# Kernel optimization log

Measured on AMD Instinct MI355X. Metric: run time of the kernel, lower is better.

## Reference

```python
import jax, jax.numpy as jnp
import numpy as np

B, L, E, H, V, NC = 64, 256, 300, 128, 50000, 2
NH1, F1 = 8, 8  # GAT layer 1: 8 heads x 8 features; layer 2: 1 head x 1 feature
LRELU = 0.2


def _lstm_dir(x, W, U, b):
    # x: [B, L, E]; W: [4H, E]; U: [4H, H]; b: [4H] (b_ih + b_hh fused)
    Bq, Hq = x.shape[0], U.shape[1]
    def step(carry, xt):
        h, c = carry
        g = xt @ W.T + h @ U.T + b
        i, f, gg, o = jnp.split(g, 4, axis=-1)  # PyTorch gate order i,f,g,o
        c = jax.nn.sigmoid(f) * c + jax.nn.sigmoid(i) * jnp.tanh(gg)
        h = jax.nn.sigmoid(o) * jnp.tanh(c)
        return (h, c), h
    h0 = jnp.zeros((Bq, Hq), x.dtype)
    _, hs = jax.lax.scan(step, (h0, h0), jnp.swapaxes(x, 0, 1))
    return jnp.swapaxes(hs, 0, 1)  # [B, L, H]


def bilstm(x, Wf, Uf, bf, Wb, Ub, bb):
    hf = _lstm_dir(x, Wf, Uf, bf)
    hb = _lstm_dir(x[:, ::-1], Wb, Ub, bb)[:, ::-1]
    return jnp.concatenate([hf, hb], axis=-1)  # [B, L, 2H]


def gat_layer(x, W, a_src, a_trg, bias, n_heads, f_out, concat, elu_act):
    # Dense equivalent of GAT IMP3 on a fully-connected graph (edge (s,t): src=s, trg=t).
    Bq, Lq, _ = x.shape
    proj = (x @ W.T).reshape(Bq, Lq, n_heads, f_out)        # [B,L,NH,F]
    s_src = jnp.einsum('blhf,hf->blh', proj, a_src)          # [B,L,NH]
    s_trg = jnp.einsum('blhf,hf->blh', proj, a_trg)
    sc = jax.nn.leaky_relu(s_src[:, :, None, :] + s_trg[:, None, :, :], LRELU)  # [B,S,T,NH]
    m = jnp.max(sc, axis=(1, 2, 3), keepdims=True)           # global max per graph (as in IMP3)
    e = jnp.exp(sc - m)
    A = e / (jnp.sum(e, axis=1, keepdims=True) + 1e-16)      # softmax over sources per target
    out = jnp.einsum('bsth,bshf->bthf', A, proj)             # scatter-aggregate to targets
    if concat:
        out = out.reshape(Bq, Lq, n_heads * f_out)
    else:
        out = out.mean(axis=2)
    out = out + bias
    if elu_act:
        out = jax.nn.elu(out)
    return out, A


def setup_inputs() -> dict:
    key = jax.random.key(0)
    ks = jax.random.split(key, 20)
    n = lambda k, shape, s=0.05: (jax.random.normal(k, shape, jnp.float32) * s)
    return {
        'input_ids': jax.random.randint(ks[0], (B, L), 0, V, jnp.int32),
        'attention_mask': jnp.ones((B, L), bool),
        'emb': n(ks[1], (V, E), 0.1),
        'Wih_f': n(ks[2], (4 * H, E)), 'Whh_f': n(ks[3], (4 * H, H)), 'b_f': jnp.zeros((4 * H,), jnp.float32),
        'Wih_b': n(ks[4], (4 * H, E)), 'Whh_b': n(ks[5], (4 * H, H)), 'b_b': jnp.zeros((4 * H,), jnp.float32),
        'g1_W': n(ks[6], (NH1 * F1, 2 * H)), 'g1_src': n(ks[7], (NH1, F1), 0.1), 'g1_trg': n(ks[8], (NH1, F1), 0.1), 'g1_b': jnp.zeros((NH1 * F1,), jnp.float32),
        'g2_W': n(ks[9], (1, NH1 * F1)), 'g2_src': n(ks[10], (1, 1), 0.1), 'g2_trg': n(ks[11], (1, 1), 0.1), 'g2_b': jnp.zeros((1,), jnp.float32),
        'ctx': n(ks[12], (L, 1), 0.1),
        'lin_W': n(ks[13], (B, 2 * H)), 'lin_b': jnp.zeros((B,), jnp.float32),
        'out_W': n(ks[14], (NC, B)), 'out_b': jnp.zeros((NC,), jnp.float32),
    }


def reference(input_ids, attention_mask, emb, Wih_f, Whh_f, b_f, Wih_b, Whh_b, b_b,
              g1_W, g1_src, g1_trg, g1_b, g2_W, g2_src, g2_trg, g2_b,
              ctx, lin_W, lin_b, out_W, out_b):
    x = emb[input_ids]                                   # [B,L,E] (dropout = eval no-op)
    h_seq = bilstm(x, Wih_f, Whh_f, b_f, Wih_b, Whh_b, b_b)  # [B,L,2H]
    h1, _ = gat_layer(h_seq, g1_W, g1_src, g1_trg, g1_b, NH1, F1, True, True)
    _, A2 = gat_layer(h1, g2_W, g2_src, g2_trg, g2_b, 1, 1, False, False)
    att2 = A2[..., 0]                                    # [B, src, trg] == att.view(-1, 2H) rows
    att = jnp.einsum('bst,t->bs', att2, ctx[:, 0])       # mm with context_vector
    att = jnp.where(attention_mask, att, -jnp.inf)
    att = jax.nn.softmax(att, axis=1)                    # [B,L]
    pooled = jnp.max(h_seq * att[..., None], axis=1)     # [B,2H]
    hcl = jax.nn.relu(pooled @ lin_W.T + lin_b)
    logits = hcl @ out_W.T + out_b                       # [B,NC]
    return (logits, att)
```

## Files before the change

kernel.cpp:

```cpp
#include <hip/hip_runtime.h>
#include <math.h>
#include <stdint.h>

#define Bq 64
#define Lq 256
#define Eq 300
#define Hq 128
#define MQ (Bq*Lq)
#define AST 320

#define LRELU_S 0.2f

__device__ __forceinline__ float lrelu(float x) { return x > 0.f ? x : LRELU_S * x; }

typedef short short8 __attribute__((ext_vector_type(8)));
typedef float f32x4v __attribute__((ext_vector_type(4)));

__device__ __forceinline__ unsigned short f2bf(float x) {
  unsigned u = __float_as_uint(x);
  u += 0x7FFFu + ((u >> 16) & 1u);
  return (unsigned short)(u >> 16);
}
__device__ __forceinline__ float bf2f(unsigned short h) {
  return __uint_as_float(((unsigned)h) << 16);
}

__device__ __forceinline__ void cv4(float4 v, unsigned short* dh, unsigned short* dl) {
  unsigned short h0 = f2bf(v.x), h1 = f2bf(v.y), h2 = f2bf(v.z), h3 = f2bf(v.w);
  unsigned short l0 = f2bf(v.x - bf2f(h0)), l1 = f2bf(v.y - bf2f(h1));
  unsigned short l2 = f2bf(v.z - bf2f(h2)), l3 = f2bf(v.w - bf2f(h3));
  uint2 ph; ph.x = (unsigned)h0 | ((unsigned)h1 << 16); ph.y = (unsigned)h2 | ((unsigned)h3 << 16);
  uint2 pl; pl.x = (unsigned)l0 | ((unsigned)l1 << 16); pl.y = (unsigned)l2 | ((unsigned)l3 << 16);
  *(uint2*)dh = ph;
  *(uint2*)dl = pl;
}

__global__ __launch_bounds__(256) void gather_conv_kernel(
    const float* __restrict__ emb, const int* __restrict__ ids,
    unsigned short* __restrict__ Agh, unsigned short* __restrict__ Agl)
{
  const int JOBS = MQ * 80;
  for (int j = blockIdx.x * blockDim.x + threadIdx.x; j < JOBS;
       j += gridDim.x * blockDim.x) {
    int row = j / 80, c = j - row * 80;
    size_t off = (size_t)row * AST + c * 4;
    if (c < 75) {
      float4 v = *(const float4*)(emb + (size_t)ids[row] * Eq + c * 4);
      cv4(v, Agh + off, Agl + off);
    } else {
      *(uint2*)(Agh + off) = make_uint2(0u, 0u);
      *(uint2*)(Agl + off) = make_uint2(0u, 0u);
    }
  }
}

__global__ __launch_bounds__(256) void conv_w_kernel(
    const float* __restrict__ Wf, const float* __restrict__ Wb,
    const float* __restrict__ g1_W,
    unsigned short* __restrict__ Wbh, unsigned short* __restrict__ Wbl,
    unsigned short* __restrict__ g1h, unsigned short* __restrict__ g1l)
{
  const int J1 = 1024 * 80;
  const int J2 = 64 * 64;
  for (int j = blockIdx.x * blockDim.x + threadIdx.x; j < J1 + J2;
       j += gridDim.x * blockDim.x) {
    if (j < J1) {
      int row = j / 80, c = j - row * 80;
      size_t off = (size_t)row * AST + c * 4;
      if (c < 75) {
        const float* src = (row < 512) ? (Wf + (size_t)row * 300)
                                       : (Wb + (size_t)(row - 512) * 300);
        float4 v = *(const float4*)(src + c * 4);
        cv4(v, Wbh + off, Wbl + off);
      } else {
        *(uint2*)(Wbh + off) = make_uint2(0u, 0u);
        *(uint2*)(Wbl + off) = make_uint2(0u, 0u);
      }
    } else {
      int j2 = j - J1;
      int row = j2 >> 6, c = j2 & 63;
      size_t off = (size_t)row * 256 + c * 4;
      float4 v = *(const float4*)(g1_W + off);
      cv4(v, g1h + off, g1l + off);
    }
  }
}

__global__ __launch_bounds__(256) void gemm_gates_mfma(
    const unsigned short* __restrict__ Agh, const unsigned short* __restrict__ Agl,
    const unsigned short* __restrict__ Wbh, const unsigned short* __restrict__ Wbl,
    const float* __restrict__ bf, const float* __restrict__ bb_,
    float* __restrict__ C)
{
  __shared__ __align__(16) short Ah[128 * 32];
  __shared__ __align__(16) short Al[128 * 32];
  __shared__ __align__(16) short Bh[128 * 32];
  __shared__ __align__(16) short Bl[128 * 32];

  int tid = threadIdx.x;
  int row0 = blockIdx.x * 128;
  int col0 = blockIdx.y * 128;
  const float* bias = (col0 < 512) ? bf : bb_;
  int wcol0 = col0 & 511;

  int l  = tid & 63, wv = tid >> 6;
  int wm = wv >> 1,  wn = wv & 1;
  int kq = l >> 4,   rl = l & 15;

  f32x4v acc[4][4] = {};

  for (int k0 = 0; k0 < 300; k0 += 32) {
    #pragma unroll
    for (int p = 0; p < 4; ++p) {
      int idx = p * 256 + tid;
      int row = idx >> 3, c4 = idx & 7;
      int gk = k0 + c4 * 4;
      int chunk = (c4 >> 1) ^ ((row >> 2) & 3);
      int off = row * 32 + chunk * 8 + (c4 & 1) * 4;
      size_t ao = (size_t)(row0 + row) * AST + gk;
      *(uint2*)&Ah[off] = *(const uint2*)(Agh + ao);
      *(uint2*)&Al[off] = *(const uint2*)(Agl + ao);
      size_t bo = (size_t)(col0 + row) * AST + gk;
      *(uint2*)&Bh[off] = *(const uint2*)(Wbh + bo);
      *(uint2*)&Bl[off] = *(const uint2*)(Wbl + bo);
    }
    __syncthreads();

    short8 ah[4], al_[4], bh[4], bl[4];
    #pragma unroll
    for (int f = 0; f < 4; ++f) {
      int ar = wm * 64 + f * 16 + rl;
      int ac = kq ^ ((ar >> 2) & 3);
      ah[f]  = *(const short8*)&Ah[ar * 32 + ac * 8];
      al_[f] = *(const short8*)&Al[ar * 32 + ac * 8];
      int br = wn * 64 + f * 16 + rl;
      int bc = kq ^ ((br >> 2) & 3);
      bh[f]  = *(const short8*)&Bh[br * 32 + bc * 8];
      bl[f]  = *(const short8*)&Bl[br * 32 + bc * 8];
    }
    #pragma unroll
    for (int fm = 0; fm < 4; ++fm)
      #pragma unroll
      for (int fn = 0; fn < 4; ++fn) {
        acc[fm][fn] = __builtin_amdgcn_mfma_f32_16x16x32_bf16(ah[fm],  bh[fn], acc[fm][fn], 0, 0, 0);
        acc[fm][fn] = __builtin_amdgcn_mfma_f32_16x16x32_bf16(ah[fm],  bl[fn], acc[fm][fn], 0, 0, 0);
        acc[fm][fn] = __builtin_amdgcn_mfma_f32_16x16x32_bf16(al_[fm], bh[fn], acc[fm][fn], 0, 0, 0);
      }
    __syncthreads();
  }

  int fq = l >> 4;
  #pragma unroll
  for (int fm = 0; fm < 4; ++fm) {
    #pragma unroll
    for (int fn = 0; fn < 4; ++fn) {
      int gr = row0 + wm * 64 + fm * 16 + fq * 4;
      int lc = wn * 64 + fn * 16 + rl;
      float bsv = bias[wcol0 + lc];
      #pragma unroll
      for (int i = 0; i < 4; ++i)
        C[(size_t)(gr + i) * 1024 + col0 + lc] = acc[fm][fn][i] + bsv;
    }
  }
}

__global__ __launch_bounds__(256) void gemm_proj_mfma(
    const unsigned short* __restrict__ Hbh, const unsigned short* __restrict__ Hbl,
    const unsigned short* __restrict__ g1h, const unsigned short* __restrict__ g1l,
    float* __restrict__ C)
{
  __shared__ __align__(16) short Ah[128 * 32];
  __shared__ __align__(16) short Al[128 * 32];
  __shared__ __align__(16) short Bh[64 * 32];
  __shared__ __align__(16) short Bl[64 * 32];

  int tid = threadIdx.x;
  int row0 = blockIdx.x * 128;

  int l  = tid & 63, wv = tid >> 6;
  int wm = wv >> 1,  wn = wv & 1;
  int kq = l >> 4,   rl = l & 15;

  f32x4v acc[4][2] = {};

  for (int k0 = 0; k0 < 256; k0 += 32) {
    #pragma unroll
    for (int p = 0; p < 4; ++p) {
      int idx = p * 256 + tid;
      int row = idx >> 3, c4 = idx & 7;
      int gk = k0 + c4 * 4;
      int chunk = (c4 >> 1) ^ ((row >> 2) & 3);
      int off = row * 32 + chunk * 8 + (c4 & 1) * 4;
      size_t ao = (size_t)(row0 + row) * 256 + gk;
      *(uint2*)&Ah[off] = *(const uint2*)(Hbh + ao);
      *(uint2*)&Al[off] = *(const uint2*)(Hbl + ao);
    }
    #pragma unroll
    for (int p = 0; p < 2; ++p) {
      int idx = p * 256 + tid;
      int row = idx >> 3, c4 = idx & 7;
      int gk = k0 + c4 * 4;
      int chunk = (c4 >> 1) ^ ((row >> 2) & 3);
      int off = row * 32 + chunk * 8 + (c4 & 1) * 4;
      size_t bo = (size_t)row * 256 + gk;
      *(uint2*)&Bh[off] = *(const uint2*)(g1h + bo);
      *(uint2*)&Bl[off] = *(const uint2*)(g1l + bo);
    }
    __syncthreads();

    short8 ah[4], al_[4], bh[2], bl[2];
    #pragma unroll
    for (int f = 0; f < 4; ++f) {
      int ar = wm * 64 + f * 16 + rl;
      int ac = kq ^ ((ar >> 2) & 3);
      ah[f]  = *(const short8*)&Ah[ar * 32 + ac * 8];
      al_[f] = *(const short8*)&Al[ar * 32 + ac * 8];
    }
    #pragma unroll
    for (int f = 0; f < 2; ++f) {
      int br = wn * 32 + f * 16 + rl;
      int bc = kq ^ ((br >> 2) & 3);
      bh[f]  = *(const short8*)&Bh[br * 32 + bc * 8];
      bl[f]  = *(const short8*)&Bl[br * 32 + bc * 8];
    }
    #pragma unroll
    for (int fm = 0; fm < 4; ++fm)
      #pragma unroll
      for (int fn = 0; fn < 2; ++fn) {
        acc[fm][fn] = __builtin_amdgcn_mfma_f32_16x16x32_bf16(ah[fm],  bh[fn], acc[fm][fn], 0, 0, 0);
        acc[fm][fn] = __builtin_amdgcn_mfma_f32_16x16x32_bf16(ah[fm],  bl[fn], acc[fm][fn], 0, 0, 0);
        acc[fm][fn] = __builtin_amdgcn_mfma_f32_16x16x32_bf16(al_[fm], bh[fn], acc[fm][fn], 0, 0, 0);
      }
    __syncthreads();
  }

  int fq = l >> 4;
  #pragma unroll
  for (int fm = 0; fm < 4; ++fm) {
    #pragma unroll
    for (int fn = 0; fn < 2; ++fn) {
      int gr = row0 + wm * 64 + fm * 16 + fq * 4;
      int lc = wn * 32 + fn * 16 + rl;
      #pragma unroll
      for (int i = 0; i < 4; ++i)
        C[(size_t)(gr + i) * 64 + lc] = acc[fm][fn][i];
    }
  }
}

#define MVB(s0,s1,s2,s3, u0,u1,u2,u3, off) \
  "s_waitcnt lgkmcnt(5)\n" \
  "v_fmac_f32 v88, v" #s0 ", v" #u0 "\n" \
  "v_fmac_f32 v89, v" #s1 ", v" #u1 "\n" \
  "v_fmac_f32 v90, v" #s2 ", v" #u2 "\n" \
  "v_fmac_f32 v91, v" #s3 ", v" #u3 "\n" \
  "ds_read_b128 v[" #s0 ":" #s3 "], v81 offset:" #off "\n"

#define MVT(n, s0,s1,s2,s3, u0,u1,u2,u3) \
  "s_waitcnt lgkmcnt(" #n ")\n" \
  "v_fmac_f32 v88, v" #s0 ", v" #u0 "\n" \
  "v_fmac_f32 v89, v" #s1 ", v" #u1 "\n" \
  "v_fmac_f32 v90, v" #s2 ", v" #u2 "\n" \
  "v_fmac_f32 v91, v" #s3 ", v" #u3 "\n"

#define ULD(lo,hi,off) \
  "global_load_dwordx4 v[" #lo ":" #hi "], v80, %[ub] offset:" #off "\n"

__global__ __launch_bounds__(512, 1) void lstm_kernel(
    const float* __restrict__ ws_base,
    const float* __restrict__ Uf, const float* __restrict__ Ub,
    float* __restrict__ h_seq,
    unsigned short* __restrict__ Hbh, unsigned short* __restrict__ Hbl)
{
  __shared__ __align__(1024) float h_sh[2][Hq];
  int blk = blockIdx.x;
  int b = blk & 63;
  int dir = blk >> 6;
  int j = threadIdx.x;
  int lane = j & 63;
  int w = j >> 6;
  int gate = (lane >> 4) & 3;
  int hidx = (w << 4) | (lane & 15);
  int row = (gate << 7) | hidx;

  const float* U = dir ? Ub : Uf;
  int tt0 = dir ? (Lq - 1) : 0;

  unsigned uo  = (unsigned)row * (Hq * 4u);
  unsigned go0 = (1024u + (unsigned)(b * Lq + tt0) * 1024u
                  + (unsigned)dir * 512u + (unsigned)row) * 4u;
  unsigned ho0 = ((unsigned)(b * Lq + tt0) * 256u
                  + (unsigned)dir * (unsigned)Hq + (unsigned)hidx) * 4u;
  unsigned hb0 = ((unsigned)(b * Lq + tt0) * 256u
                  + (unsigned)dir * (unsigned)Hq + (unsigned)hidx) * 2u;
  int gd  = dir ? -4096 : 4096;
  int hd  = dir ? -1024 : 1024;
  int hdb = dir ? -512  : 512;

  unsigned lds_base = (unsigned)(uintptr_t)&h_sh[0][0];
  unsigned ldsr0 = lds_base;
  unsigned ldsw0 = lds_base + 512u + (unsigned)hidx * 4u;

  bool isg = (gate == 2);
  float klog = isg ? -2.8853900817779268f : -1.4426950408889634f;
  float mc = isg ? 2.f : 1.f;
  float ac = isg ? -1.f : 0.f;
  int base4 = (lane & 15) * 4;
  int bp0 = base4, bp1 = base4 + 64, bp2 = base4 + 128, bp3 = base4 + 192;

  if (j < Hq) h_sh[0][j] = 0.f;
  __syncthreads();

  asm volatile(
    "v_mov_b32 v80, %[uo]\n"
    "v_mov_b32 v81, %[ldsr0]\n"
    "v_mov_b32 v82, %[ldsw0]\n"
    "v_mov_b32 v83, %[go0]\n"
    "v_mov_b32 v84, %[ho0]\n"
    "v_mov_b32 v74, %[hb0]\n"
    "v_mov_b32 v87, 0\n"
    "s_mov_b32 s90, 0\n"
    ULD(128,131,0)   ULD(132,135,16)  ULD(136,139,32)  ULD(140,143,48)
    ULD(144,147,64)  ULD(148,151,80)  ULD(152,155,96)  ULD(156,159,112)
    ULD(160,163,128) ULD(164,167,144) ULD(168,171,160) ULD(172,175,176)
    ULD(176,179,192) ULD(180,183,208) ULD(184,187,224) ULD(188,191,240)
    ULD(192,195,256) ULD(196,199,272) ULD(200,203,288) ULD(204,207,304)
    ULD(208,211,320) ULD(212,215,336) ULD(216,219,352) ULD(220,223,368)
    ULD(224,227,384) ULD(228,231,400) ULD(232,235,416) ULD(236,239,432)
    ULD(240,243,448) ULD(244,247,464) ULD(248,251,480) ULD(252,255,496)
    "global_load_dword v85, v83, %[wsb]\n"
    "s_waitcnt vmcnt(0)\n"
    "Ltop_%=:\n"
    "v_add_u32 v83, %[gd], v83\n"
    "global_load_dword v86, v83, %[wsb]\n"
    "ds_read_b128 v[100:103], v81\n"
    "ds_read_b128 v[104:107], v81 offset:16\n"
    "ds_read_b128 v[108:111], v81 offset:32\n"
    "ds_read_b128 v[112:115], v81 offset:48\n"
    "ds_read_b128 v[116:119], v81 offset:64\n"
    "ds_read_b128 v[120:123], v81 offset:80\n"
    "v_mov_b32 v88, v85\n"
    "v_mov_b32 v89, 0\n"
    "v_mov_b32 v90, 0\n"
    "v_mov_b32 v91, 0\n"
    MVB(100,101,102,103, 128,129,130,131, 96)
    MVB(104,105,106,107, 132,133,134,135, 112)
    MVB(108,109,110,111, 136,137,138,139, 128)
    MVB(112,113,114,115, 140,141,142,143, 144)
    MVB(116,117,118,119, 144,145,146,147, 160)
    MVB(120,121,122,123, 148,149,150,151, 176)
    MVB(100,101,102,103, 152,153,154,155, 192)
    MVB(104,105,106,107, 156,157,158,159, 208)
    MVB(108,109,110,111, 160,161,162,163, 224)
    MVB(112,113,114,115, 164,165,166,167, 240)
    MVB(116,117,118,119, 168,169,170,171, 256)
    MVB(120,121,122,123, 172,173,174,175, 272)
    MVB(100,101,102,103, 176,177,178,179, 288)
    MVB(104,105,106,107, 180,181,182,183, 304)
    MVB(108,109,110,111, 184,185,186,187, 320)
    MVB(112,113,114,115, 188,189,190,191, 336)
    MVB(116,117,118,119, 192,193,194,195, 352)
    MVB(120,121,122,123, 196,197,198,199, 368)
    MVB(100,101,102,103, 200,201,202,203, 384)
    MVB(104,105,106,107, 204,205,206,207, 400)
    MVB(108,109,110,111, 208,209,210,211, 416)
    MVB(112,113,114,115, 212,213,214,215, 432)
    MVB(116,117,118,119, 216,217,218,219, 448)
    MVB(120,121,122,123, 220,221,222,223, 464)
    MVB(100,101,102,103, 224,225,226,227, 480)
    MVB(104,105,106,107, 228,229,230,231, 496)
    MVT(5, 108,109,110,111, 232,233,234,235)
    MVT(4, 112,113,114,115, 236,237,238,239)
    MVT(3, 116,117,118,119, 240,241,242,243)
    MVT(2, 120,121,122,123, 244,245,246,247)
    MVT(1, 100,101,102,103, 248,249,250,251)
    MVT(0, 104,105,106,107, 252,253,254,255)
    "v_add_f32 v88, v88, v90\n"
    "v_add_f32 v89, v89, v91\n"
    "v_add_f32 v88, v88, v89\n"
    "v_mul_f32 v92, %[klog], v88\n"
    "v_exp_f32 v93, v92\n"
    "s_nop 1\n"
    "v_add_f32 v94, 1.0, v93\n"
    "v_rcp_f32 v95, v94\n"
    "s_nop 1\n"
    "v_fma_f32 v97, v95, %[mc], %[ac]\n"
    "ds_bpermute_b32 v92, %[bp0], v97\n"
    "ds_bpermute_b32 v93, %[bp1], v97\n"
    "ds_bpermute_b32 v94, %[bp2], v97\n"
    "ds_bpermute_b32 v98, %[bp3], v97\n"
    "s_waitcnt lgkmcnt(0)\n"
    "v_mul_f32 v95, v92, v94\n"
    "v_fma_f32 v87, v93, v87, v95\n"
    "v_mul_f32 v92, 0xc038aa3b, v87\n"
    "v_exp_f32 v93, v92\n"
    "s_nop 1\n"
    "v_add_f32 v94, 1.0, v93\n"
    "v_rcp_f32 v95, v94\n"
    "s_nop 1\n"
    "v_fma_f32 v96, v95, 2.0, -1.0\n"
    "v_mul_f32 v96, v98, v96\n"
    "v_bfe_u32 v75, v96, 16, 1\n"
    "v_add_u32 v75, 0x7fff, v75\n"
    "v_add_u32 v76, v96, v75\n"
    "v_lshrrev_b32 v77, 16, v76\n"
    "v_lshlrev_b32 v78, 16, v77\n"
    "v_sub_f32 v78, v96, v78\n"
    "v_bfe_u32 v75, v78, 16, 1\n"
    "v_add_u32 v75, 0x7fff, v75\n"
    "v_add_u32 v79, v78, v75\n"
    "v_lshrrev_b32 v79, 16, v79\n"
    "s_waitcnt vmcnt(0)\n"
    "v_mov_b32 v85, v86\n"
    "ds_write_b32 v82, v96\n"
    "global_store_dword v84, v96, %[hsb]\n"
    "global_store_short v74, v77, %[hbh]\n"
    "global_store_short v74, v79, %[hbl]\n"
    "v_add_u32 v84, %[hd], v84\n"
    "v_add_u32 v74, %[hdb], v74\n"
    "v_xor_b32 v81, 0x200, v81\n"
    "v_xor_b32 v82, 0x200, v82\n"
    "s_waitcnt lgkmcnt(0)\n"
    "s_barrier\n"
    "s_add_u32 s90, s90, 1\n"
    "s_cmp_lt_u32 s90, 256\n"
    "s_cbranch_scc1 Ltop_%=\n"
    "s_waitcnt vmcnt(0) lgkmcnt(0)\n"
    :
    : [wsb]"s"(ws_base), [hsb]"s"(h_seq), [ub]"s"(U),
      [hbh]"s"(Hbh), [hbl]"s"(Hbl),
      [gd]"s"(gd), [hd]"s"(hd), [hdb]"s"(hdb),
      [uo]"v"(uo), [go0]"v"(go0), [ho0]"v"(ho0), [hb0]"v"(hb0),
      [ldsr0]"v"(ldsr0), [ldsw0]"v"(ldsw0),
      [klog]"v"(klog), [mc]"v"(mc), [ac]"v"(ac),
      [bp0]"v"(bp0), [bp1]"v"(bp1), [bp2]"v"(bp2), [bp3]"v"(bp3)
    : "memory", "scc", "s90",
      "v74","v75","v76","v77","v78","v79",
      "v80","v81","v82","v83","v84","v85","v86","v87","v88","v89",
      "v90","v91","v92","v93","v94","v95","v96","v97","v98",
      "v100","v101","v102","v103","v104","v105","v106","v107",
      "v108","v109","v110","v111","v112","v113","v114","v115",
      "v116","v117","v118","v119","v120","v121","v122","v123",
      "v128","v129","v130","v131","v132","v133","v134","v135",
      "v136","v137","v138","v139","v140","v141","v142","v143",
      "v144","v145","v146","v147","v148","v149","v150","v151",
      "v152","v153","v154","v155","v156","v157","v158","v159",
      "v160","v161","v162","v163","v164","v165","v166","v167",
      "v168","v169","v170","v171","v172","v173","v174","v175",
      "v176","v177","v178","v179","v180","v181","v182","v183",
      "v184","v185","v186","v187","v188","v189","v190","v191",
      "v192","v193","v194","v195","v196","v197","v198","v199",
      "v200","v201","v202","v203","v204","v205","v206","v207",
      "v208","v209","v210","v211","v212","v213","v214","v215",
      "v216","v217","v218","v219","v220","v221","v222","v223",
      "v224","v225","v226","v227","v228","v229","v230","v231",
      "v232","v233","v234","v235","v236","v237","v238","v239",
      "v240","v241","v242","v243","v244","v245","v246","v247",
      "v248","v249","v250","v251","v252","v253","v254","v255");
}
#undef MVB
#undef MVT
#undef ULD

__device__ __forceinline__ float block_max_256(float v, volatile float* red) {
  #pragma unroll
  for (int o = 32; o > 0; o >>= 1) v = fmaxf(v, __shfl_xor(v, o, 64));
  int tid = threadIdx.x;
  if ((tid & 63) == 0) red[tid >> 6] = v;
  __syncthreads();
  float r = fmaxf(fmaxf(red[0], red[1]), fmaxf(red[2], red[3]));
  __syncthreads();
  return r;
}
__device__ __forceinline__ float block_sum_256(float v, volatile float* red) {
  #pragma unroll
  for (int o = 32; o > 0; o >>= 1) v += __shfl_xor(v, o, 64);
  int tid = threadIdx.x;
  if ((tid & 63) == 0) red[tid >> 6] = v;
  __syncthreads();
  float r = red[0] + red[1] + red[2] + red[3];
  __syncthreads();
  return r;
}

__global__ __launch_bounds__(256) void gat1_fused_kernel(
    const float* __restrict__ proj1, const float* __restrict__ g1_src,
    const float* __restrict__ g1_trg, const float* __restrict__ g1_b,
    float* __restrict__ h1)
{
  int b = blockIdx.x >> 3;
  int h = blockIdx.x & 7;
  int t = threadIdx.x;
  __shared__ float src_s[Lq], trg_s[Lq];
  __shared__ float proj_s[Lq * 8];
  __shared__ float red[4];

  size_t base = (size_t)b * Lq;
  float pv[8];
  {
    const float4* pr = (const float4*)(proj1 + (base + t) * 64 + h * 8);
    float4 p0 = pr[0], p1 = pr[1];
    pv[0]=p0.x; pv[1]=p0.y; pv[2]=p0.z; pv[3]=p0.w;
    pv[4]=p1.x; pv[5]=p1.y; pv[6]=p1.z; pv[7]=p1.w;
    float4* psh = (float4*)(proj_s + t * 8);
    psh[0] = p0; psh[1] = p1;
  }
  float ss = 0.f, st = 0.f;
  #pragma unroll
  for (int f = 0; f < 8; ++f) {
    ss += pv[f] * g1_src[h * 8 + f];
    st += pv[f] * g1_trg[h * 8 + f];
  }
  src_s[t] = ss;
  trg_s[t] = st;
  __syncthreads();

  float ms = block_max_256(ss, red);
  float mt = block_max_256(st, red);
  float m = lrelu(ms + mt);

  float mytrg = trg_s[t];
  float den = 1e-16f;
  float acc[8] = {};
  for (int s = 0; s < Lq; ++s) {
    float wgt = __expf(lrelu(src_s[s] + mytrg) - m);
    den += wgt;
    const float* ps = proj_s + s * 8;
    #pragma unroll
    for (int f = 0; f < 8; ++f) acc[f] += wgt * ps[f];
  }
  float inv = 1.f / den;
  float* out = h1 + (base + t) * 64 + h * 8;
  #pragma unroll
  for (int f = 0; f < 8; ++f) {
    float v = acc[f] * inv + g1_b[h * 8 + f];
    out[f] = v > 0.f ? v : expm1f(v);
  }
}

__global__ __launch_bounds__(256) void gat2_pool_head_kernel(
    const float* __restrict__ h1, const float* __restrict__ g2_W,
    const float* __restrict__ g2_src, const float* __restrict__ g2_trg,
    const float* __restrict__ ctx, const float* __restrict__ h_seq,
    const float* __restrict__ lin_W, const float* __restrict__ lin_b,
    const float* __restrict__ out_W, const float* __restrict__ out_b,
    float* __restrict__ att_out, float* __restrict__ logits)
{
  int b = blockIdx.x;
  int tid = threadIdx.x;
  __shared__ float w2[64];
  __shared__ float src2[Lq], trg2[Lq], dq[Lq], att_sh[Lq], pool_sh[256];
  __shared__ float red[4];
  __shared__ float part[4][64];
  __shared__ float hcl[64];

  if (tid < 64) w2[tid] = g2_W[tid];
  __syncthreads();

  const float* hr = h1 + ((size_t)b * Lq + tid) * 64;
  float p = 0.f;
  #pragma unroll
  for (int k = 0; k < 64; ++k) p += hr[k] * w2[k];
  float a_s = g2_src[0], a_t = g2_trg[0];
  src2[tid] = p * a_s;
  trg2[tid] = p * a_t;
  __syncthreads();

  float ms = block_max_256(src2[tid], red);
  float mt = block_max_256(trg2[tid], red);
  float m2 = lrelu(ms + mt);

  float mytrg = trg2[tid];
  float d0 = 1e-16f, d1 = 0.f, d2 = 0.f, d3 = 0.f;
  for (int s = 0; s < Lq; s += 4) {
    d0 += __expf(lrelu(src2[s + 0] + mytrg) - m2);
    d1 += __expf(lrelu(src2[s + 1] + mytrg) - m2);
    d2 += __expf(lrelu(src2[s + 2] + mytrg) - m2);
    d3 += __expf(lrelu(src2[s + 3] + mytrg) - m2);
  }
  dq[tid] = ctx[tid] / ((d0 + d1) + (d2 + d3));
  __syncthreads();

  float mysrc = src2[tid];
  float r0 = 0.f, r1 = 0.f, r2 = 0.f, r3 = 0.f;
  for (int t = 0; t < Lq; t += 4) {
    r0 += dq[t + 0] * __expf(lrelu(mysrc + trg2[t + 0]) - m2);
    r1 += dq[t + 1] * __expf(lrelu(mysrc + trg2[t + 1]) - m2);
    r2 += dq[t + 2] * __expf(lrelu(mysrc + trg2[t + 2]) - m2);
    r3 += dq[t + 3] * __expf(lrelu(mysrc + trg2[t + 3]) - m2);
  }
  float raw = (r0 + r1) + (r2 + r3);

  float mr = block_max_256(raw, red);
  float e = __expf(raw - mr);
  float ssum = block_sum_256(e, red);
  float att = e / ssum;
  att_out[(size_t)b * Lq + tid] = att;
  att_sh[tid] = att;
  __syncthreads();

  float pm = -3.4e38f;
  const float* hb = h_seq + (size_t)b * Lq * 256 + tid;
  for (int l = 0; l < Lq; l += 4) {
    float v0 = hb[(size_t)(l + 0) * 256] * att_sh[l + 0];
    float v1 = hb[(size_t)(l + 1) * 256] * att_sh[l + 1];
    float v2 = hb[(size_t)(l + 2) * 256] * att_sh[l + 2];
    float v3 = hb[(size_t)(l + 3) * 256] * att_sh[l + 3];
    pm = fmaxf(pm, fmaxf(fmaxf(v0, v1), fmaxf(v2, v3)));
  }
  pool_sh[tid] = pm;
  __syncthreads();

  {
    int jj = tid & 63, kq = tid >> 6;
    const float* pr = pool_sh + kq * 64;
    const float* wr = lin_W + jj * 256 + kq * 64;
    float d = 0.f;
    #pragma unroll
    for (int k = 0; k < 64; ++k) d += pr[k] * wr[k];
    part[kq][jj] = d;
  }
  __syncthreads();
  if (tid < 64) {
    float v = part[0][tid] + part[1][tid] + part[2][tid] + part[3][tid] + lin_b[tid];
    hcl[tid] = fmaxf(v, 0.f);
  }
  __syncthreads();
  if (tid < 128) {
    int cc = tid >> 6, jj = tid & 63;
    float pp = hcl[jj] * out_W[cc * 64 + jj];
    #pragma unroll
    for (int o = 32; o > 0; o >>= 1) pp += __shfl_xor(pp, o, 64);
    if (jj == 0) logits[b * 2 + cc] = pp + out_b[cc];
  }
}

extern "C" void kernel_launch(void* const* d_in, const int* in_sizes, int n_in,
                              void* d_out, int out_size, void* d_ws, size_t ws_size,
                              hipStream_t stream)
{
  const int*   ids    = (const int*)  d_in[0];
  const float* emb    = (const float*)d_in[2];
  const float* Wih_f  = (const float*)d_in[3];
  const float* Whh_f  = (const float*)d_in[4];
  const float* b_f    = (const float*)d_in[5];
  const float* Wih_b  = (const float*)d_in[6];
  const float* Whh_b  = (const float*)d_in[7];
  const float* b_b    = (const float*)d_in[8];
  const float* g1_W   = (const float*)d_in[9];
  const float* g1_src = (const float*)d_in[10];
  const float* g1_trg = (const float*)d_in[11];
  const float* g1_b   = (const float*)d_in[12];
  const float* g2_W   = (const float*)d_in[13];
  const float* g2_src = (const float*)d_in[14];
  const float* g2_trg = (const float*)d_in[15];
  const float* ctx    = (const float*)d_in[17];
  const float* lin_W  = (const float*)d_in[18];
  const float* lin_b  = (const float*)d_in[19];
  const float* out_W  = (const float*)d_in[20];
  const float* out_b  = (const float*)d_in[21];

  float* out_f   = (float*)d_out;
  float* logits  = out_f;
  float* att_out = out_f + 128;

  float* ws = (float*)d_ws;
  const size_t M = MQ;
  float* ws_base = ws;
  ws += 1024;
  float* gates   = ws; ws += M * 1024;
  float* h_seq   = ws; ws += M * 256;
  float* proj1   = ws; ws += M * 64;
  float* h1      = ws; ws += M * 64;
  unsigned short* Agh = (unsigned short*)ws; ws += M * AST / 2;
  unsigned short* Agl = (unsigned short*)ws; ws += M * AST / 2;
  unsigned short* Wbh = (unsigned short*)ws; ws += 1024 * AST / 2;
  unsigned short* Wbl = (unsigned short*)ws; ws += 1024 * AST / 2;
  unsigned short* g1h = (unsigned short*)ws; ws += 64 * 256 / 2;
  unsigned short* g1l = (unsigned short*)ws; ws += 64 * 256 / 2;
  unsigned short* Hbh = (unsigned short*)ws; ws += M * 256 / 2;
  unsigned short* Hbl = (unsigned short*)ws; ws += M * 256 / 2;

  dim3 thr(256);

  gather_conv_kernel<<<2048, thr, 0, stream>>>(emb, ids, Agh, Agl);
  conv_w_kernel<<<512, thr, 0, stream>>>(Wih_f, Wih_b, g1_W, Wbh, Wbl, g1h, g1l);

  gemm_gates_mfma<<<dim3(MQ / 128, 1024 / 128), thr, 0, stream>>>(Agh, Agl, Wbh, Wbl, b_f, b_b, gates);

  lstm_kernel<<<128, 512, 0, stream>>>(ws_base, Whh_f, Whh_b, h_seq, Hbh, Hbl);

  gemm_proj_mfma<<<MQ / 128, thr, 0, stream>>>(Hbh, Hbl, g1h, g1l, proj1);
  gat1_fused_kernel<<<Bq * 8, thr, 0, stream>>>(proj1, g1_src, g1_trg, g1_b, h1);

  gat2_pool_head_kernel<<<Bq, thr, 0, stream>>>(h1, g2_W, g2_src, g2_trg, ctx, h_seq,
                                                lin_W, lin_b, out_W, out_b,
                                                att_out, logits);
}
```

Measured before the change: 307.8 us.

## Drop fp32 h_seq store, pool from bf16 hi/lo pairs, merge conversion kernels

New measurement: 303.6 us. Within noise of the previous version (-1.3%).

```diff
diff --git a/kernel.cpp b/kernel.cpp
--- a/kernel.cpp
+++ b/kernel.cpp
@@ -35,37 +35,32 @@
   *(uint2*)dl = pl;
 }
 
-__global__ __launch_bounds__(256) void gather_conv_kernel(
+__global__ __launch_bounds__(256) void conv_all_kernel(
     const float* __restrict__ emb, const int* __restrict__ ids,
-    unsigned short* __restrict__ Agh, unsigned short* __restrict__ Agl)
-{
-  const int JOBS = MQ * 80;
-  for (int j = blockIdx.x * blockDim.x + threadIdx.x; j < JOBS;
-       j += gridDim.x * blockDim.x) {
-    int row = j / 80, c = j - row * 80;
-    size_t off = (size_t)row * AST + c * 4;
-    if (c < 75) {
-      float4 v = *(const float4*)(emb + (size_t)ids[row] * Eq + c * 4);
-      cv4(v, Agh + off, Agl + off);
-    } else {
-      *(uint2*)(Agh + off) = make_uint2(0u, 0u);
-      *(uint2*)(Agl + off) = make_uint2(0u, 0u);
-    }
-  }
-}
-
-__global__ __launch_bounds__(256) void conv_w_kernel(
     const float* __restrict__ Wf, const float* __restrict__ Wb,
     const float* __restrict__ g1_W,
+    unsigned short* __restrict__ Agh, unsigned short* __restrict__ Agl,
     unsigned short* __restrict__ Wbh, unsigned short* __restrict__ Wbl,
     unsigned short* __restrict__ g1h, unsigned short* __restrict__ g1l)
 {
+  const int JA = MQ * 80;
   const int J1 = 1024 * 80;
   const int J2 = 64 * 64;
-  for (int j = blockIdx.x * blockDim.x + threadIdx.x; j < J1 + J2;
+  for (int j = blockIdx.x * blockDim.x + threadIdx.x; j < JA + J1 + J2;
        j += gridDim.x * blockDim.x) {
-    if (j < J1) {
+    if (j < JA) {
       int row = j / 80, c = j - row * 80;
+      size_t off = (size_t)row * AST + c * 4;
+      if (c < 75) {
+        float4 v = *(const float4*)(emb + (size_t)ids[row] * Eq + c * 4);
+        cv4(v, Agh + off, Agl + off);
+      } else {
+        *(uint2*)(Agh + off) = make_uint2(0u, 0u);
+        *(uint2*)(Agl + off) = make_uint2(0u, 0u);
+      }
+    } else if (j < JA + J1) {
+      int j1 = j - JA;
+      int row = j1 / 80, c = j1 - row * 80;
       size_t off = (size_t)row * AST + c * 4;
       if (c < 75) {
         const float* src = (row < 512) ? (Wf + (size_t)row * 300)
@@ -77,7 +72,7 @@
         *(uint2*)(Wbl + off) = make_uint2(0u, 0u);
       }
     } else {
-      int j2 = j - J1;
+      int j2 = j - JA - J1;
       int row = j2 >> 6, c = j2 & 63;
       size_t off = (size_t)row * 256 + c * 4;
       float4 v = *(const float4*)(g1_W + off);
@@ -269,7 +264,6 @@
 __global__ __launch_bounds__(512, 1) void lstm_kernel(
     const float* __restrict__ ws_base,
     const float* __restrict__ Uf, const float* __restrict__ Ub,
-    float* __restrict__ h_seq,
     unsigned short* __restrict__ Hbh, unsigned short* __restrict__ Hbl)
 {
   __shared__ __align__(1024) float h_sh[2][Hq];
@@ -289,12 +283,9 @@
   unsigned uo  = (unsigned)row * (Hq * 4u);
   unsigned go0 = (1024u + (unsigned)(b * Lq + tt0) * 1024u
                   + (unsigned)dir * 512u + (unsigned)row) * 4u;
-  unsigned ho0 = ((unsigned)(b * Lq + tt0) * 256u
-                  + (unsigned)dir * (unsigned)Hq + (unsigned)hidx) * 4u;
   unsigned hb0 = ((unsigned)(b * Lq + tt0) * 256u
                   + (unsigned)dir * (unsigned)Hq + (unsigned)hidx) * 2u;
   int gd  = dir ? -4096 : 4096;
-  int hd  = dir ? -1024 : 1024;
   int hdb = dir ? -512  : 512;
 
   unsigned lds_base = (unsigned)(uintptr_t)&h_sh[0][0];
@@ -316,7 +307,6 @@
     "v_mov_b32 v81, %[ldsr0]\n"
     "v_mov_b32 v82, %[ldsw0]\n"
     "v_mov_b32 v83, %[go0]\n"
-    "v_mov_b32 v84, %[ho0]\n"
     "v_mov_b32 v74, %[hb0]\n"
     "v_mov_b32 v87, 0\n"
     "s_mov_b32 s90, 0\n"
@@ -400,23 +390,15 @@
     "s_nop 1\n"
     "v_fma_f32 v96, v95, 2.0, -1.0\n"
     "v_mul_f32 v96, v98, v96\n"
-    "v_bfe_u32 v75, v96, 16, 1\n"
-    "v_add_u32 v75, 0x7fff, v75\n"
-    "v_add_u32 v76, v96, v75\n"
-    "v_lshrrev_b32 v77, 16, v76\n"
+    "v_cvt_pk_bf16_f32 v77, v96, v96\n"
     "v_lshlrev_b32 v78, 16, v77\n"
     "v_sub_f32 v78, v96, v78\n"
-    "v_bfe_u32 v75, v78, 16, 1\n"
-    "v_add_u32 v75, 0x7fff, v75\n"
-    "v_add_u32 v79, v78, v75\n"
-    "v_lshrrev_b32 v79, 16, v79\n"
+    "v_cvt_pk_bf16_f32 v79, v78, v78\n"
     "s_waitcnt vmcnt(0)\n"
     "v_mov_b32 v85, v86\n"
     "ds_write_b32 v82, v96\n"
-    "global_store_dword v84, v96, %[hsb]\n"
     "global_store_short v74, v77, %[hbh]\n"
     "global_store_short v74, v79, %[hbl]\n"
-    "v_add_u32 v84, %[hd], v84\n"
     "v_add_u32 v74, %[hdb], v74\n"
     "v_xor_b32 v81, 0x200, v81\n"
     "v_xor_b32 v82, 0x200, v82\n"
@@ -427,16 +409,16 @@
     "s_cbranch_scc1 Ltop_%=\n"
     "s_waitcnt vmcnt(0) lgkmcnt(0)\n"
     :
-    : [wsb]"s"(ws_base), [hsb]"s"(h_seq), [ub]"s"(U),
+    : [wsb]"s"(ws_base), [ub]"s"(U),
       [hbh]"s"(Hbh), [hbl]"s"(Hbl),
-      [gd]"s"(gd), [hd]"s"(hd), [hdb]"s"(hdb),
-      [uo]"v"(uo), [go0]"v"(go0), [ho0]"v"(ho0), [hb0]"v"(hb0),
+      [gd]"s"(gd), [hdb]"s"(hdb),
+      [uo]"v"(uo), [go0]"v"(go0), [hb0]"v"(hb0),
       [ldsr0]"v"(ldsr0), [ldsw0]"v"(ldsw0),
       [klog]"v"(klog), [mc]"v"(mc), [ac]"v"(ac),
       [bp0]"v"(bp0), [bp1]"v"(bp1), [bp2]"v"(bp2), [bp3]"v"(bp3)
     : "memory", "scc", "s90",
-      "v74","v75","v76","v77","v78","v79",
-      "v80","v81","v82","v83","v84","v85","v86","v87","v88","v89",
+      "v74","v77","v78","v79",
+      "v80","v81","v82","v83","v85","v86","v87","v88","v89",
       "v90","v91","v92","v93","v94","v95","v96","v97","v98",
       "v100","v101","v102","v103","v104","v105","v106","v107",
       "v108","v109","v110","v111","v112","v113","v114","v115",
@@ -541,7 +523,8 @@
 __global__ __launch_bounds__(256) void gat2_pool_head_kernel(
     const float* __restrict__ h1, const float* __restrict__ g2_W,
     const float* __restrict__ g2_src, const float* __restrict__ g2_trg,
-    const float* __restrict__ ctx, const float* __restrict__ h_seq,
+    const float* __restrict__ ctx,
+    const unsigned short* __restrict__ Hbh, const unsigned short* __restrict__ Hbl,
     const float* __restrict__ lin_W, const float* __restrict__ lin_b,
     const float* __restrict__ out_W, const float* __restrict__ out_b,
     float* __restrict__ att_out, float* __restrict__ logits)
@@ -600,12 +583,17 @@
   __syncthreads();
 
   float pm = -3.4e38f;
-  const float* hb = h_seq + (size_t)b * Lq * 256 + tid;
+  const unsigned short* ph = Hbh + (size_t)b * Lq * 256 + tid;
+  const unsigned short* pl = Hbl + (size_t)b * Lq * 256 + tid;
   for (int l = 0; l < Lq; l += 4) {
-    float v0 = hb[(size_t)(l + 0) * 256] * att_sh[l + 0];
-    float v1 = hb[(size_t)(l + 1) * 256] * att_sh[l + 1];
-    float v2 = hb[(size_t)(l + 2) * 256] * att_sh[l + 2];
-    float v3 = hb[(size_t)(l + 3) * 256] * att_sh[l + 3];
+    float h0 = bf2f(ph[(size_t)(l + 0) * 256]) + bf2f(pl[(size_t)(l + 0) * 256]);
+    float h1v = bf2f(ph[(size_t)(l + 1) * 256]) + bf2f(pl[(size_t)(l + 1) * 256]);
+    float h2 = bf2f(ph[(size_t)(l + 2) * 256]) + bf2f(pl[(size_t)(l + 2) * 256]);
+    float h3 = bf2f(ph[(size_t)(l + 3) * 256]) + bf2f(pl[(size_t)(l + 3) * 256]);
+    float v0 = h0 * att_sh[l + 0];
+    float v1 = h1v * att_sh[l + 1];
+    float v2 = h2 * att_sh[l + 2];
+    float v3 = h3 * att_sh[l + 3];
     pm = fmaxf(pm, fmaxf(fmaxf(v0, v1), fmaxf(v2, v3)));
   }
   pool_sh[tid] = pm;
@@ -669,7 +657,6 @@
   float* ws_base = ws;
   ws += 1024;
   float* gates   = ws; ws += M * 1024;
-  float* h_seq   = ws; ws += M * 256;
   float* proj1   = ws; ws += M * 64;
   float* h1      = ws; ws += M * 64;
   unsigned short* Agh = (unsigned short*)ws; ws += M * AST / 2;
@@ -683,17 +670,18 @@
 
   dim3 thr(256);
 
-  gather_conv_kernel<<<2048, thr, 0, stream>>>(emb, ids, Agh, Agl);
-  conv_w_kernel<<<512, thr, 0, stream>>>(Wih_f, Wih_b, g1_W, Wbh, Wbl, g1h, g1l);
+  conv_all_kernel<<<2048, thr, 0, stream>>>(emb, ids, Wih_f, Wih_b, g1_W,
+                                            Agh, Agl, Wbh, Wbl, g1h, g1l);
 
   gemm_gates_mfma<<<dim3(MQ / 128, 1024 / 128), thr, 0, stream>>>(Agh, Agl, Wbh, Wbl, b_f, b_b, gates);
 
-  lstm_kernel<<<128, 512, 0, stream>>>(ws_base, Whh_f, Whh_b, h_seq, Hbh, Hbl);
+  lstm_kernel<<<128, 512, 0, stream>>>(ws_base, Whh_f, Whh_b, Hbh, Hbl);
 
   gemm_proj_mfma<<<MQ / 128, thr, 0, stream>>>(Hbh, Hbl, g1h, g1l, proj1);
   gat1_fused_kernel<<<Bq * 8, thr, 0, stream>>>(proj1, g1_src, g1_trg, g1_b, h1);
 
-  gat2_pool_head_kernel<<<Bq, thr, 0, stream>>>(h1, g2_W, g2_src, g2_trg, ctx, h_seq,
+  gat2_pool_head_kernel<<<Bq, thr, 0, stream>>>(h1, g2_W, g2_src, g2_trg, ctx,
+                                                Hbh, Hbl,
                                                 lin_W, lin_b, out_W, out_b,
                                                 att_out, logits);
 }
```
